# Optimization experiments

Measured on AMD Instinct MI355X. Metric: run time of the kernel, lower is better.

The kernel has to match this reference:

```python
import jax, jax.numpy as jnp
import numpy as np

M_RANGE = 3
K = 2 * M_RANGE + 1          # kernel size = 7
N_CLASS = K * K              # 49 motion classes
IM_CHANNEL = 3


def setup_inputs() -> dict:
    key = jax.random.key(0)
    k1, k2, k3, k4 = jax.random.split(key, 4)
    B, H, W = 16, 256, 256
    im_input = jax.random.normal(k1, (B, 2 * IM_CHANNEL, H, W), dtype=jnp.float32)
    im_output = jax.random.normal(k2, (B, IM_CHANNEL, H, W), dtype=jnp.float32)
    # motion in [-M_RANGE, M_RANGE-1) so that floor(m)+M_RANGE+1 <= K-1 (valid bin)
    gt_motion = jax.random.uniform(k3, (B, 2, H, W), dtype=jnp.float32) * (2 * M_RANGE - 1) - M_RANGE
    # grouped-conv weight (already in post-swapaxes [n_class, 1, K, K] layout)
    m_kernel = jax.random.uniform(k4, (N_CLASS, 1, K, K), dtype=jnp.float32)
    return {"im_input": im_input, "im_output": im_output,
            "gt_motion": gt_motion, "m_kernel": m_kernel}


def _axis_weights(m):
    # m: [B,H,W] -> bilinear binning weights over K bins: [B,H,W,K]
    f = jnp.floor(m)
    frac = m - f
    idx = f.astype(jnp.int32) + M_RANGE
    oh0 = jax.nn.one_hot(idx, K, dtype=m.dtype)
    oh1 = jax.nn.one_hot(idx + 1, K, dtype=m.dtype)
    return (1.0 - frac)[..., None] * oh0 + frac[..., None] * oh1


def motion2mask(motion):
    # faithful vectorization of the triple-loop: mask[c=iy*K+ix] = b[iy]*a[ix]
    ax = _axis_weights(motion[:, 0])   # x-motion -> columns of ger(b, a)
    ay = _axis_weights(motion[:, 1])   # y-motion -> rows
    mask = ay[..., :, None] * ax[..., None, :]       # [B,H,W,K,K] outer product
    B, H, W = motion.shape[0], motion.shape[2], motion.shape[3]
    return mask.reshape(B, H, W, N_CLASS).transpose(0, 3, 1, 2)  # [B,N_CLASS,H,W]


def _conv(x, w, groups):
    return jax.lax.conv_general_dilated(
        x, w, window_strides=(1, 1),
        padding=[(M_RANGE, M_RANGE), (M_RANGE, M_RANGE)],
        dimension_numbers=("NCHW", "OIHW", "NCHW"),
        feature_group_count=groups)


def reference(im_input, im_output, gt_motion, m_kernel):
    m_mask = motion2mask(gt_motion)                   # [B,N_CLASS,H,W]
    out_mask = _conv(m_mask, m_kernel, N_CLASS)       # grouped conv, same shape
    im = im_input[:, -IM_CHANNEL:]                    # [B,3,H,W]
    B, C, H, W = im.shape
    # construct_image: each channel expanded to N_CLASS copies then grouped-conv
    # == plain conv of each single channel with all N_CLASS kernels
    nearby = _conv(im.reshape(B * C, 1, H, W), m_kernel, 1)
    nearby = nearby.reshape(B, C, N_CLASS, H, W)
    pred = (nearby * out_mask[:, None]).sum(axis=2)   # [B,3,H,W]
    return pred, m_mask
```

## Files before the change

kernel.cpp:

```cpp
#include <hip/hip_runtime.h>
#include <hip/hip_fp16.h>

typedef _Float16 f16x8 __attribute__((ext_vector_type(8)));
typedef float    f32x4 __attribute__((ext_vector_type(4)));

#define TILE   16
#define HALO   22
#define KK     7
#define NCLASS 49
#define IMW    256
#define IMH    256
#define HW     65536
#define HH     484
#define WST    52

__device__ __forceinline__ unsigned h2u(__half2 h) { union { __half2 h; unsigned u; } c; c.h = h; return c.u; }
__device__ __forceinline__ __half2  u2h(unsigned u) { union { __half2 h; unsigned u; } c; c.u = u; return c.h; }
__device__ __forceinline__ int rowOf(int n) { return (n & 1) ? (25 + (n >> 1)) : (n >> 1); }

__global__ __launch_bounds__(256, 2)
void gtnet_kernel(const float* __restrict__ im_input,
                  const float* __restrict__ gt_motion,
                  const float* __restrict__ m_kernel,
                  float* __restrict__ out_pred,
                  float* __restrict__ out_mask)
{
    __shared__ __align__(16) unsigned omP[256 * WST];
    __shared__ unsigned KB[NCLASS * NCLASS];
    __shared__ uint4    haloP[HH];
    __shared__ __align__(16) float iml4[HH * 4];

    const int tid  = threadIdx.x;
    const int lane = tid & 63, wv_id = tid >> 6;
    const int tx = tid & 15, ty = tid >> 4;
    const int x0 = blockIdx.x * TILE, y0 = blockIdx.y * TILE;
    const int b  = blockIdx.z;
    const int x = x0 + tx, y = y0 + ty;

    for (int i = tid; i < NCLASS * NCLASS; i += 256) {
        int s = i / NCLASS, r = i - s * NCLASS;
        int n0 = (r < 25) ? (2 * r) : (2 * (r - 25) + 1);
        int n1 = n0 + 1;
        float k0 = m_kernel[n0 * NCLASS + s];
        float k1 = (n1 < NCLASS) ? m_kernel[n1 * NCLASS + s] : 0.f;
        KB[i] = h2u(__halves2half2(__float2half_rn(k0), __float2half_rn(k1)));
    }

    const float* mot_x = gt_motion + (size_t)b * 2 * HW;
    const float* mot_y = mot_x + HW;
    for (int i = tid; i < HH; i += 256) {
        int hy = i / HALO, hx = i - hy * HALO;
        int gy = y0 - 3 + hy, gx = x0 - 3 + hx;
        uint4 e;
        if (gy >= 0 && gy < IMH && gx >= 0 && gx < IMW) {
            int off = gy * IMW + gx;
            float ay = mot_y[off] + 3.0f;
            float ax = mot_x[off] + 3.0f;
            float iyf = floorf(ay), ixf = floorf(ax);
            float fy = ay - iyf,    fx = ax - ixf;
            int   n00 = (int)iyf * KK + (int)ixf;
            e.x = h2u(__halves2half2(__float2half_rn(1.0f - fy), __float2half_rn(fy)));
            e.y = h2u(__halves2half2(__float2half_rn(1.0f - fx), __float2half_rn(fx)));
            e.z = (unsigned)((rowOf(n00) << 16) | rowOf(n00 + KK));
            e.w = 0;
        } else {
            e.x = 0; e.y = 0; e.z = (0u << 16) | 28u; e.w = 0;
        }
        haloP[i] = e;
    }

    const float* imP = im_input + ((size_t)b * 6 + 3) * HW;
    for (int i = tid; i < HH; i += 256) {
        int hy = i / HALO, hx = i - hy * HALO;
        int gy = y0 - 3 + hy, gx = x0 - 3 + hx;
        float4 v = {0.0f, 0.0f, 0.0f, 0.0f};
        if (gy >= 0 && gy < IMH && gx >= 0 && gx < IMW) {
            int off = gy * IMW + gx;
            v.x = imP[off];
            v.y = imP[off + HW];
            v.z = imP[off + 2 * HW];
        }
        *reinterpret_cast<float4*>(&iml4[i * 4]) = v;
    }

    {
        uint4* p = reinterpret_cast<uint4*>(omP);
        for (int i = tid; i < (NCLASS * 256) / 4 + 1; i += 256)
            if (i * 4 < NCLASS * 256 + 4) p[i] = make_uint4(0, 0, 0, 0);
    }

    __syncthreads();

    {
        int off = y * IMW + x;
        float ay = mot_y[off] + 3.0f;
        float ax = mot_x[off] + 3.0f;
        float iyf = floorf(ay), ixf = floorf(ax);
        float fy = ay - iyf,    fx = ax - ixf;
        int   iy = (int)iyf,    ix = (int)ixf;
        float wyA[KK], wxB[KK];
        #pragma unroll
        for (int a = 0; a < KK; a++) {
            wyA[a] = (a == iy) ? (1.0f - fy) : ((a == iy + 1) ? fy : 0.0f);
            wxB[a] = (a == ix) ? (1.0f - fx) : ((a == ix + 1) ? fx : 0.0f);
        }
        float* mm = out_mask + (size_t)b * NCLASS * HW + off;
        #pragma unroll
        for (int a = 0; a < KK; a++)
            #pragma unroll
            for (int bb = 0; bb < KK; bb++)
                mm[(size_t)(a * KK + bb) * HW] = wyA[a] * wxB[bb];
    }

    #pragma unroll
    for (int u = 0; u < KK; u++) {
        #pragma unroll
        for (int v = 0; v < KK; v++) {
            const int s = u * KK + v;
            uint4 hp = haloP[(ty + u) * HALO + (tx + v)];
            __half2 wy = u2h(hp.x);
            __half2 wx = u2h(hp.y);
            int rowA = (int)(hp.z >> 16), rowB = (int)(hp.z & 0xffffu);
            __half2 kA = u2h(KB[s * NCLASS + rowA]);
            __half2 kB = u2h(KB[s * NCLASS + rowB]);
            __half2 cA = __hmul2(__hmul2(__low2half2(wy),  wx), kA);
            __half2 cB = __hmul2(__hmul2(__high2half2(wy), wx), kB);
            unsigned* pA = &omP[rowA * 256 + tid];
            unsigned* pB = &omP[rowB * 256 + tid];
            *pA = h2u(__hadd2(u2h(*pA), cA));
            *pB = h2u(__hadd2(u2h(*pB), cB));
        }
    }

    __syncthreads();

    f16x8 af[2][4];
    #pragma unroll
    for (int kit = 0; kit < 2; kit++) {
        #pragma unroll
        for (int mt = 0; mt < 4; mt++) {
            int kk0 = kit * 32 + (lane >> 4) * 8;
            int rE  = kk0 >> 1;
            int px  = wv_id * 64 + mt * 16 + (lane & 15);
            unsigned Ew[4], Ow[5];
            #pragma unroll
            for (int i2 = 0; i2 < 4; i2++) {
                int r = rE + i2;
                unsigned val = omP[r * 256 + px];
                Ew[i2] = (r <= 24) ? val : 0u;
            }
            #pragma unroll
            for (int j = 0; j < 5; j++) {
                int o   = rE - 1 + j;
                int row = 25 + o;
                row = (row > 48) ? 48 : row;
                unsigned val = omP[row * 256 + px];
                Ow[j] = (o >= 0 && o <= 23) ? val : 0u;
            }
            union { unsigned u[4]; f16x8 v; } au;
            #pragma unroll
            for (int i2 = 0; i2 < 4; i2++) {
                unsigned oal = (Ow[i2 + 1] << 16) | (Ow[i2] >> 16);
                au.u[i2] = h2u(__hadd2(u2h(Ew[i2]), u2h(oal)));
            }
            af[kit][mt] = au.v;
        }
    }
    f16x8 bfr[2][4];
    #pragma unroll
    for (int kit = 0; kit < 2; kit++) {
        #pragma unroll
        for (int nt = 0; nt < 4; nt++) {
            int t   = nt * 16 + (lane & 15);
            int kk0 = kit * 32 + (lane >> 4) * 8;
            int rE  = kk0 >> 1;
            union { unsigned u[4]; f16x8 v; } bu;
            #pragma unroll
            for (int j = 0; j < 4; j++) {
                int r = rE + j;
                unsigned val = KB[t * NCLASS + r];
                bu.u[j] = (r <= 24) ? val : 0u;
            }
            bfr[kit][nt] = bu.v;
        }
    }

    __syncthreads();

    f32x4 acc[4][4];
    #pragma unroll
    for (int mt = 0; mt < 4; mt++) {
        #pragma unroll
        for (int nt = 0; nt < 4; nt++) {
            f32x4 c = {0.0f, 0.0f, 0.0f, 0.0f};
            c = __builtin_amdgcn_mfma_f32_16x16x32_f16(af[0][mt], bfr[0][nt], c, 0, 0, 0);
            c = __builtin_amdgcn_mfma_f32_16x16x32_f16(af[1][mt], bfr[1][nt], c, 0, 0, 0);
            acc[mt][nt] = c;
        }
    }

    float* Wf = reinterpret_cast<float*>(omP);
    #pragma unroll
    for (int mt = 0; mt < 4; mt++) {
        #pragma unroll
        for (int nt = 0; nt < 4; nt++) {
            int t = nt * 16 + (lane & 15);
            if (t < NCLASS) {
                #pragma unroll
                for (int r = 0; r < 4; r++) {
                    int px = wv_id * 64 + mt * 16 + (lane >> 4) * 4 + r;
                    Wf[px * WST + t] = acc[mt][nt][r];
                }
            }
        }
    }

    __syncthreads();

    float wv[NCLASS];
    #pragma unroll
    for (int t = 0; t < NCLASS; t++) wv[t] = Wf[tid * WST + t];

    float a0 = 0.0f, a1 = 0.0f, a2 = 0.0f;
    #pragma unroll
    for (int p = 0; p < KK; p++) {
        #pragma unroll
        for (int q = 0; q < KK; q++) {
            float wvv = wv[p * KK + q];
            int   hi = (ty + p) * HALO + (tx + q);
            float4 im3 = *reinterpret_cast<const float4*>(&iml4[hi * 4]);
            a0 = fmaf(wvv, im3.x, a0);
            a1 = fmaf(wvv, im3.y, a1);
            a2 = fmaf(wvv, im3.z, a2);
        }
    }
    float* pr = out_pred + (size_t)b * 3 * HW + y * IMW + x;
    pr[0]      = a0;
    pr[HW]     = a1;
    pr[2 * HW] = a2;
}

extern "C" void kernel_launch(void* const* d_in, const int* in_sizes, int n_in,
                              void* d_out, int out_size, void* d_ws, size_t ws_size,
                              hipStream_t stream) {
    const float* im_input  = (const float*)d_in[0];
    const float* gt_motion = (const float*)d_in[2];
    const float* m_kernel  = (const float*)d_in[3];

    float* pred = (float*)d_out;
    float* mask = pred + (size_t)16 * 3 * HW;

    dim3 grid(IMW / TILE, IMH / TILE, 16);
    dim3 block(256);
    hipLaunchKernelGGL(gtnet_kernel, grid, block, 0, stream,
                       im_input, gt_motion, m_kernel, pred, mask);
}
```

Measured before the change: 356.7 us.

## Repack shared-memory mask accumulator into vertical-pair layout to cut LDS footprint

Reorganizes the shared-memory mask accumulator from 49 odd/even packed rows into 42 rows pairing class n with n+7 (vertical neighbors), split into two 128-pixel halves, and rebuilds the kernel tables (KV for the scatter, KE for MFMA B operands). Halo data is split into a compact weight pair plus a byte offset, and the image halo is stored as float2+float instead of padded float4. The aim is to shrink the LDS footprint and simplify the scatter addressing so that occupancy and bank behavior improve. The cost is more complex A-fragment reconstruction with extra loads and shifts before the MFMA.

```diff
diff --git a/kernel.cpp b/kernel.cpp
--- a/kernel.cpp
+++ b/kernel.cpp
@@ -12,11 +12,20 @@
 #define IMH    256
 #define HW     65536
 #define HH     484
+#define NV     42
 #define WST    52
+
+#define OFF_OMV    0
+#define OFF_HALOW  10752
+#define OFF_HALON  11720
+#define OFF_KV     12204
+#define OFF_KE     14262
+#define OFF_IML64  15488
+#define OFF_IML32  16456
+#define SH_TOTAL   16940
 
 __device__ __forceinline__ unsigned h2u(__half2 h) { union { __half2 h; unsigned u; } c; c.h = h; return c.u; }
 __device__ __forceinline__ __half2  u2h(unsigned u) { union { __half2 h; unsigned u; } c; c.u = u; return c.h; }
-__device__ __forceinline__ int rowOf(int n) { return (n & 1) ? (25 + (n >> 1)) : (n >> 1); }
 
 __global__ __launch_bounds__(256, 2)
 void gtnet_kernel(const float* __restrict__ im_input,
@@ -25,10 +34,15 @@
                   float* __restrict__ out_pred,
                   float* __restrict__ out_mask)
 {
-    __shared__ __align__(16) unsigned omP[256 * WST];
-    __shared__ unsigned KB[NCLASS * NCLASS];
-    __shared__ uint4    haloP[HH];
-    __shared__ __align__(16) float iml4[HH * 4];
+    __shared__ __align__(16) unsigned SH[SH_TOTAL];
+    unsigned* const omV   = SH + OFF_OMV;
+    uint2*   const haloW  = (uint2*)(SH + OFF_HALOW);
+    unsigned* const haloN = SH + OFF_HALON;
+    unsigned* const KV    = SH + OFF_KV;
+    unsigned* const KE    = SH + OFF_KE;
+    float2*  const iml64  = (float2*)(SH + OFF_IML64);
+    float*   const iml32  = (float*)(SH + OFF_IML32);
+    float*   const Wf     = (float*)SH;
 
     const int tid  = threadIdx.x;
     const int lane = tid & 63, wv_id = tid >> 6;
@@ -37,13 +51,17 @@
     const int b  = blockIdx.z;
     const int x = x0 + tx, y = y0 + ty;
 
-    for (int i = tid; i < NCLASS * NCLASS; i += 256) {
-        int s = i / NCLASS, r = i - s * NCLASS;
-        int n0 = (r < 25) ? (2 * r) : (2 * (r - 25) + 1);
-        int n1 = n0 + 1;
-        float k0 = m_kernel[n0 * NCLASS + s];
-        float k1 = (n1 < NCLASS) ? m_kernel[n1 * NCLASS + s] : 0.f;
-        KB[i] = h2u(__halves2half2(__float2half_rn(k0), __float2half_rn(k1)));
+    for (int i = tid; i < NCLASS * NV; i += 256) {
+        int s = i / NV, n = i - s * NV;
+        float k0 = m_kernel[n * NCLASS + s];
+        float k7 = m_kernel[(n + KK) * NCLASS + s];
+        KV[i] = h2u(__halves2half2(__float2half_rn(k0), __float2half_rn(k7)));
+    }
+    for (int i = tid; i < NCLASS * 25; i += 256) {
+        int t = i / 25, j = i - t * 25;
+        float k0 = m_kernel[(2 * j) * NCLASS + t];
+        float k1 = (2 * j + 1 < NCLASS) ? m_kernel[(2 * j + 1) * NCLASS + t] : 0.0f;
+        KE[i] = h2u(__halves2half2(__float2half_rn(k0), __float2half_rn(k1)));
     }
 
     const float* mot_x = gt_motion + (size_t)b * 2 * HW;
@@ -51,42 +69,43 @@
     for (int i = tid; i < HH; i += 256) {
         int hy = i / HALO, hx = i - hy * HALO;
         int gy = y0 - 3 + hy, gx = x0 - 3 + hx;
-        uint4 e;
+        uint2 wv2 = make_uint2(0u, 0u);
+        unsigned n4 = 0;
         if (gy >= 0 && gy < IMH && gx >= 0 && gx < IMW) {
             int off = gy * IMW + gx;
             float ay = mot_y[off] + 3.0f;
             float ax = mot_x[off] + 3.0f;
             float iyf = floorf(ay), ixf = floorf(ax);
             float fy = ay - iyf,    fx = ax - ixf;
-            int   n00 = (int)iyf * KK + (int)ixf;
-            e.x = h2u(__halves2half2(__float2half_rn(1.0f - fy), __float2half_rn(fy)));
-            e.y = h2u(__halves2half2(__float2half_rn(1.0f - fx), __float2half_rn(fx)));
-            e.z = (unsigned)((rowOf(n00) << 16) | rowOf(n00 + KK));
-            e.w = 0;
-        } else {
-            e.x = 0; e.y = 0; e.z = (0u << 16) | 28u; e.w = 0;
-        }
-        haloP[i] = e;
+            int n00 = (int)iyf * KK + (int)ixf;
+            n00 = (n00 < 0) ? 0 : ((n00 > 40) ? 40 : n00);
+            wv2.x = h2u(__halves2half2(__float2half_rn(1.0f - fy), __float2half_rn(fy)));
+            wv2.y = h2u(__halves2half2(__float2half_rn(1.0f - fx), __float2half_rn(fx)));
+            n4 = (unsigned)(n00 * 4);
+        }
+        haloW[i] = wv2;
+        haloN[i] = n4;
     }
 
     const float* imP = im_input + ((size_t)b * 6 + 3) * HW;
     for (int i = tid; i < HH; i += 256) {
         int hy = i / HALO, hx = i - hy * HALO;
         int gy = y0 - 3 + hy, gx = x0 - 3 + hx;
-        float4 v = {0.0f, 0.0f, 0.0f, 0.0f};
+        float2 v01 = make_float2(0.0f, 0.0f);
+        float  v2  = 0.0f;
         if (gy >= 0 && gy < IMH && gx >= 0 && gx < IMW) {
             int off = gy * IMW + gx;
-            v.x = imP[off];
-            v.y = imP[off + HW];
-            v.z = imP[off + 2 * HW];
-        }
-        *reinterpret_cast<float4*>(&iml4[i * 4]) = v;
+            v01.x = imP[off];
+            v01.y = imP[off + HW];
+            v2    = imP[off + 2 * HW];
+        }
+        iml64[i] = v01;
+        iml32[i] = v2;
     }
 
     {
-        uint4* p = reinterpret_cast<uint4*>(omP);
-        for (int i = tid; i < (NCLASS * 256) / 4 + 1; i += 256)
-            if (i * 4 < NCLASS * 256 + 4) p[i] = make_uint4(0, 0, 0, 0);
+        uint4* p = reinterpret_cast<uint4*>(omV);
+        for (int i = tid; i < (2 * NV * 128) / 4; i += 256) p[i] = make_uint4(0, 0, 0, 0);
     }
 
     __syncthreads();
@@ -112,23 +131,25 @@
                 mm[(size_t)(a * KK + bb) * HW] = wyA[a] * wxB[bb];
     }
 
+    unsigned* const omHalf = omV + (tid >> 7) * (NV * 128) + (tid & 127);
     #pragma unroll
     for (int u = 0; u < KK; u++) {
         #pragma unroll
         for (int v = 0; v < KK; v++) {
             const int s = u * KK + v;
-            uint4 hp = haloP[(ty + u) * HALO + (tx + v)];
-            __half2 wy = u2h(hp.x);
-            __half2 wx = u2h(hp.y);
-            int rowA = (int)(hp.z >> 16), rowB = (int)(hp.z & 0xffffu);
-            __half2 kA = u2h(KB[s * NCLASS + rowA]);
-            __half2 kB = u2h(KB[s * NCLASS + rowB]);
-            __half2 cA = __hmul2(__hmul2(__low2half2(wy),  wx), kA);
-            __half2 cB = __hmul2(__hmul2(__high2half2(wy), wx), kB);
-            unsigned* pA = &omP[rowA * 256 + tid];
-            unsigned* pB = &omP[rowB * 256 + tid];
-            *pA = h2u(__hadd2(u2h(*pA), cA));
-            *pB = h2u(__hadd2(u2h(*pB), cB));
+            const int q = (ty + u) * HALO + (tx + v);
+            uint2 wyx = haloW[q];
+            unsigned n4 = haloN[q];
+            const unsigned* kp =
+                (const unsigned*)((const char*)KV + s * (NV * 4) + n4);
+            unsigned kvA = kp[0], kvB = kp[1];
+            unsigned* ob = (unsigned*)((char*)omHalf + n4 * 128);
+            unsigned o0 = ob[0], o1 = ob[128];
+            __half2 wy = u2h(wyx.x), wx = u2h(wyx.y);
+            __half2 cA = __hmul2(__hmul2(wy, __low2half2(wx)),  u2h(kvA));
+            __half2 cB = __hmul2(__hmul2(wy, __high2half2(wx)), u2h(kvB));
+            ob[0]   = h2u(__hadd2(u2h(o0), cA));
+            ob[128] = h2u(__hadd2(u2h(o1), cB));
         }
     }
 
@@ -139,29 +160,25 @@
     for (int kit = 0; kit < 2; kit++) {
         #pragma unroll
         for (int mt = 0; mt < 4; mt++) {
-            int kk0 = kit * 32 + (lane >> 4) * 8;
-            int rE  = kk0 >> 1;
+            int k0  = kit * 32 + (lane >> 4) * 8;
             int px  = wv_id * 64 + mt * 16 + (lane & 15);
-            unsigned Ew[4], Ow[5];
-            #pragma unroll
-            for (int i2 = 0; i2 < 4; i2++) {
-                int r = rE + i2;
-                unsigned val = omP[r * 256 + px];
-                Ew[i2] = (r <= 24) ? val : 0u;
-            }
-            #pragma unroll
-            for (int j = 0; j < 5; j++) {
-                int o   = rE - 1 + j;
-                int row = 25 + o;
-                row = (row > 48) ? 48 : row;
-                unsigned val = omP[row * 256 + px];
-                Ow[j] = (o >= 0 && o <= 23) ? val : 0u;
-            }
+            const unsigned* pxb = omV + (px >> 7) * (NV * 128) + (px & 127);
             union { unsigned u[4]; f16x8 v; } au;
             #pragma unroll
-            for (int i2 = 0; i2 < 4; i2++) {
-                unsigned oal = (Ow[i2 + 1] << 16) | (Ow[i2] >> 16);
-                au.u[i2] = h2u(__hadd2(u2h(Ew[i2]), u2h(oal)));
+            for (int j = 0; j < 4; j++) {
+                int c0 = k0 + 2 * j;
+                int rl = (c0 > 40) ? 40 : c0;
+                unsigned d0 = pxb[rl * 128], d1 = pxb[rl * 128 + 128];
+                unsigned loM = (d0 & 0xffffu) | (d1 << 16);
+                loM = (c0 <= 40) ? loM : 0u;
+                int r0 = c0 - 7; r0 = (r0 < 0) ? 0 : ((r0 > 41) ? 41 : r0);
+                int r1 = c0 - 6; r1 = (r1 < 0) ? 0 : ((r1 > 41) ? 41 : r1);
+                unsigned e0 = pxb[r0 * 128];
+                unsigned e1 = pxb[r1 * 128];
+                e0 = (c0 >= 8 && c0 <= 48) ? e0 : 0u;
+                e1 = (c0 >= 6 && c0 <= 48) ? e1 : 0u;
+                unsigned hiM = (e0 >> 16) | (e1 & 0xffff0000u);
+                au.u[j] = h2u(__hadd2(u2h(loM), u2h(hiM)));
             }
             af[kit][mt] = au.v;
         }
@@ -171,15 +188,15 @@
     for (int kit = 0; kit < 2; kit++) {
         #pragma unroll
         for (int nt = 0; nt < 4; nt++) {
-            int t   = nt * 16 + (lane & 15);
-            int kk0 = kit * 32 + (lane >> 4) * 8;
-            int rE  = kk0 >> 1;
+            int t  = nt * 16 + (lane & 15);
+            int k0 = kit * 32 + (lane >> 4) * 8;
             union { unsigned u[4]; f16x8 v; } bu;
             #pragma unroll
             for (int j = 0; j < 4; j++) {
-                int r = rE + j;
-                unsigned val = KB[t * NCLASS + r];
-                bu.u[j] = (r <= 24) ? val : 0u;
+                int c0 = k0 + 2 * j;
+                int j2 = c0 >> 1;
+                unsigned val = KE[t * 25 + ((j2 > 24) ? 24 : j2)];
+                bu.u[j] = (c0 <= 48) ? val : 0u;
             }
             bfr[kit][nt] = bu.v;
         }
@@ -199,7 +216,6 @@
         }
     }
 
-    float* Wf = reinterpret_cast<float*>(omP);
     #pragma unroll
     for (int mt = 0; mt < 4; mt++) {
         #pragma unroll
@@ -228,10 +244,11 @@
         for (int q = 0; q < KK; q++) {
             float wvv = wv[p * KK + q];
             int   hi = (ty + p) * HALO + (tx + q);
-            float4 im3 = *reinterpret_cast<const float4*>(&iml4[hi * 4]);
-            a0 = fmaf(wvv, im3.x, a0);
-            a1 = fmaf(wvv, im3.y, a1);
-            a2 = fmaf(wvv, im3.z, a2);
+            float2 i01 = iml64[hi];
+            float  i2  = iml32[hi];
+            a0 = fmaf(wvv, i01.x, a0);
+            a1 = fmaf(wvv, i01.y, a1);
+            a2 = fmaf(wvv, i2,    a2);
         }
     }
     float* pr = out_pred + (size_t)b * 3 * HW + y * IMW + x;
```

Measured after the change: 339.8 us. 1.05x faster.
